# Optimization experiments

Measured on AMD Instinct MI355X. Metric: run time of the kernel, lower is better.

The kernel has to match this reference:

```python
import jax, jax.numpy as jnp
import numpy as np

N_HEAD = 16


def _rope(x, cos, sin):
    # x: [B, T, H, hd]; cos/sin: [1, T, 1, hd//2] (interleaved-pair rotation)
    x1, x2 = x[..., ::2], x[..., 1::2]
    r1 = x1 * cos - x2 * sin
    r2 = x1 * sin + x2 * cos
    return jnp.stack([r1, r2], axis=-1).reshape(x.shape)


def setup_inputs() -> dict:
    key = jax.random.key(0)
    k1, k2, k3 = jax.random.split(key, 3)
    B, T, D = 2, 2048, 2048
    x = jax.random.normal(k1, (B, T, D), dtype=jnp.float32)
    w_attn = jax.random.normal(k2, (3 * D, D), dtype=jnp.float32) * 0.02
    w_proj = jax.random.normal(k3, (D, D), dtype=jnp.float32) * 0.02
    return {"x": x, "w_attn": w_attn, "w_proj": w_proj}


def reference(x, w_attn, w_proj):
    B, T, D = x.shape
    H = N_HEAD
    hd = D // H
    # fused QKV projection (bias=False)
    qkv = x @ w_attn.T                      # [B, T, 3D]
    q, k, v = jnp.split(qkv, 3, axis=-1)
    q = q.reshape(B, T, H, hd)
    k = k.reshape(B, T, H, hd)
    v = v.reshape(B, T, H, hd)
    # RoPE tables: inv_freq = 1/10000^(2i/hd), angles m*theta_i
    inv_freq = 1.0 / (10000.0 ** (jnp.arange(0, hd, 2, dtype=jnp.float32) / hd))
    t = jnp.arange(T, dtype=jnp.float32)
    freqs = t[:, None] * inv_freq[None, :]  # [T, hd//2]
    cos = jnp.cos(freqs)[None, :, None, :]
    sin = jnp.sin(freqs)[None, :, None, :]
    q = _rope(q, cos, sin)
    k = _rope(k, cos, sin)
    # causal attention with materialized [B,H,T,T] scores (as in source)
    scale = 1.0 / np.sqrt(hd).astype(np.float32)
    att = jnp.einsum('bthd,bshd->bhts', q, k) * scale
    causal = jnp.tril(jnp.ones((T, T), dtype=bool))
    att = jnp.where(causal, att, -jnp.inf)
    att = jax.nn.softmax(att, axis=-1)
    y = jnp.einsum('bhts,bshd->bthd', att, v).reshape(B, T, D)
    return y @ w_proj.T
```

## Files before the change

kernel.cpp:

```cpp
#include <hip/hip_runtime.h>
#include <hip/hip_bf16.h>

#define T_SEQ 2048
#define DMODEL 2048
#define NB 2
#define NH 16
#define HD 128

typedef __attribute__((ext_vector_type(8))) short short8;
typedef __attribute__((ext_vector_type(4))) float f32x4;
typedef __attribute__((ext_vector_type(16))) float f32x16;
typedef unsigned short ushort_t;

__device__ inline ushort_t f2bf(float f) {
  union { float f; unsigned u; } v; v.f = f;
  unsigned r = v.u + 0x7fffu + ((v.u >> 16) & 1u);
  return (ushort_t)(r >> 16);
}
__device__ inline float bf2f(ushort_t u) {
  union { unsigned u; float f; } v; v.u = ((unsigned)u) << 16;
  return v.f;
}
__device__ inline unsigned pk2(float x, float y) {
  union { __hip_bfloat162 h; unsigned u; } c;
  c.h = __float22bfloat162_rn(float2{x, y});
  return c.u;
}
__device__ inline float fexp2(float x) {
  float r;
  asm("v_exp_f32 %0, %1" : "=v"(r) : "v"(x));
  return r;
}

__device__ inline void gload16(const void* g, void* l) {
  __builtin_amdgcn_global_load_lds(
      (const __attribute__((address_space(1))) unsigned*)g,
      (__attribute__((address_space(3))) unsigned*)l, 16, 0, 0);
}

__global__ void cvt_all(const float* __restrict__ x, const float* __restrict__ wa,
                        const float* __restrict__ wp, ushort_t* __restrict__ xb,
                        ushort_t* __restrict__ wab, ushort_t* __restrict__ wpb,
                        int n8x, int n8a, int n8p) {
  int i = blockIdx.x * blockDim.x + threadIdx.x;
  const float* src; ushort_t* dst; int j;
  if (i < n8x)              { src = x;  dst = xb;  j = i; }
  else if (i < n8x + n8a)   { src = wa; dst = wab; j = i - n8x; }
  else if (i < n8x + n8a + n8p) { src = wp; dst = wpb; j = i - n8x - n8a; }
  else return;
  const float4* s = (const float4*)src + (size_t)j * 2;
  float4 a = s[0], b = s[1];
  short8 o;
  o[0] = (short)f2bf(a.x); o[1] = (short)f2bf(a.y);
  o[2] = (short)f2bf(a.z); o[3] = (short)f2bf(a.w);
  o[4] = (short)f2bf(b.x); o[5] = (short)f2bf(b.y);
  o[6] = (short)f2bf(b.z); o[7] = (short)f2bf(b.w);
  *((short8*)dst + j) = o;
}

__global__ void trig_init(float* __restrict__ trig) {
  int idx = blockIdx.x * blockDim.x + threadIdx.x;
  if (idx >= T_SEQ * 64) return;
  int i = idx & 63, t = idx >> 6;
  float inv = __expf(-(float)i * (9.210340371976184f / 64.0f));
  float f = (float)t * inv;
  trig[idx * 2]     = cosf(f);
  trig[idx * 2 + 1] = sinf(f);
}

__global__ __launch_bounds__(256)
void v_transpose(const ushort_t* __restrict__ v, ushort_t* __restrict__ vt) {
  __shared__ __align__(16) ushort_t L[64][136];
  int bh = blockIdx.y;
  int t0 = blockIdx.x * 64;
  int tid = threadIdx.x;
  int row = tid >> 2, c0 = (tid & 3) * 32;
  const ushort_t* src = v + ((size_t)bh * T_SEQ + t0 + row) * HD + c0;
#pragma unroll
  for (int j = 0; j < 4; ++j)
    *(short8*)&L[row][c0 + j * 8] = *(const short8*)(src + j * 8);
  __syncthreads();
  int d = tid >> 1, tc = (tid & 1) * 32;
  union { ushort_t u[32]; short8 v8[4]; } buf;
#pragma unroll
  for (int j = 0; j < 32; ++j) buf.u[j] = L[tc + j][d];
  ushort_t* dst = vt + ((size_t)bh * HD + d) * T_SEQ + t0 + tc;
#pragma unroll
  for (int j = 0; j < 4; ++j) *(short8*)(dst + j * 8) = buf.v8[j];
}

template <int EPI>
__global__ __launch_bounds__(256, 4)
void gemm_s(const ushort_t* __restrict__ A, const ushort_t* __restrict__ Bt,
            float* __restrict__ C, ushort_t* __restrict__ q_t,
            ushort_t* __restrict__ k_t, ushort_t* __restrict__ v_t,
            const float* __restrict__ trig, int M, int N, int K) {
  __shared__ __align__(16) ushort_t sA[2][128 * 32];
  __shared__ __align__(16) ushort_t sB[2][128 * 32];
  int tid = threadIdx.x, lane = tid & 63, w = tid >> 6;
  int wm = w >> 1, wn = w & 1;
  int li = lane & 15, lg = lane >> 4;
  int tile_m = blockIdx.y * 128, tile_n = blockIdx.x * 128;
  const ushort_t* Ag = A + (size_t)tile_m * K;
  const ushort_t* Bg = Bt + (size_t)tile_n * K;

  int Rl = tid >> 3;
  int sl = tid & 7;
  int tdec = sl ^ (Rl & 7);
  int prow = (tdec >> 2) & 1, gch = tdec & 3;

  auto stage = [&](int kt, int buf) {
#pragma unroll
    for (int i = 0; i < 2; ++i) {
      int grow = (i * 32 + Rl) * 2 + prow;
      gload16(Ag + (size_t)grow * K + kt * 32 + gch * 8,
              &sA[buf][i * 2048 + tid * 8]);
    }
#pragma unroll
    for (int i = 0; i < 2; ++i) {
      int grow = (i * 32 + Rl) * 2 + prow;
      gload16(Bg + (size_t)grow * K + kt * 32 + gch * 8,
              &sB[buf][i * 2048 + tid * 8]);
    }
  };

  auto rdoff = [&](int r) {
    int R = r >> 1;
    int s = (((r & 1) << 2) | lg) ^ (R & 7);
    return R * 64 + s * 8;
  };

  f32x4 acc[4][4] = {};
  const int NT = K / 32;

  stage(0, 0);
  __syncthreads();

  for (int kt = 0; kt < NT; ++kt) {
    int cur = kt & 1;
    if (kt + 1 < NT) stage(kt + 1, cur ^ 1);
    short8 af[4], bf[4];
#pragma unroll
    for (int mi = 0; mi < 4; ++mi)
      af[mi] = *(const short8*)&sA[cur][rdoff(wm * 64 + mi * 16 + li)];
#pragma unroll
    for (int ni = 0; ni < 4; ++ni)
      bf[ni] = *(const short8*)&sB[cur][rdoff(wn * 64 + ni * 16 + li)];
    __builtin_amdgcn_s_setprio(1);
#pragma unroll
    for (int mi = 0; mi < 4; ++mi)
#pragma unroll
      for (int ni = 0; ni < 4; ++ni)
        acc[mi][ni] = __builtin_amdgcn_mfma_f32_16x16x32_bf16(af[mi], bf[ni], acc[mi][ni], 0, 0, 0);
    __builtin_amdgcn_s_setprio(0);
    __syncthreads();
  }

  if (EPI == 0) {
#pragma unroll
    for (int mi = 0; mi < 4; ++mi) {
      int trow = tile_m + wm * 64 + mi * 16 + lg * 4;
#pragma unroll
      for (int ni = 0; ni < 4; ++ni) {
        int col = tile_n + wn * 64 + ni * 16 + li;
#pragma unroll
        for (int r = 0; r < 4; ++r)
          C[(size_t)(trow + r) * N + col] = acc[mi][ni][r];
      }
    }
  } else {
    int sec = tile_n >> 11;
    int bq  = tile_m >> 11;
    int t0  = tile_m & 2047;
    int h   = (tile_n & 2047) >> 7;
#pragma unroll
    for (int mi = 0; mi < 4; ++mi) {
      int tl = wm * 64 + mi * 16 + lg * 4;
#pragma unroll
      for (int ni = 0; ni < 4; ++ni) {
        int d = wn * 64 + ni * 16 + li;
        if (sec < 2) {
          ushort_t* base = ((sec == 0) ? q_t : k_t) + ((size_t)(bq * NH + h)) * T_SEQ * HD;
          int fi2 = (d >> 1) * 2;
#pragma unroll
          for (int r = 0; r < 4; ++r) {
            int t = t0 + tl + r;
            float val = acc[mi][ni][r];
            float par = __shfl_xor(val, 1);
            const float* tp = trig + t * 128 + fi2;
            float c = tp[0], s = tp[1];
            float outv = (li & 1) ? (par * s + val * c) : (val * c - par * s);
            base[(size_t)t * HD + d] = f2bf(outv);
          }
        } else {
          ushort_t* base = v_t + ((size_t)(bq * NH + h)) * T_SEQ * HD;
#pragma unroll
          for (int r = 0; r < 4; ++r)
            base[(size_t)(t0 + tl + r) * HD + d] = f2bf(acc[mi][ni][r]);
        }
      }
    }
  }
}

__global__ __launch_bounds__(256, 2)
void flash_attn(const ushort_t* __restrict__ Q, const ushort_t* __restrict__ Kg,
                const ushort_t* __restrict__ Vt, ushort_t* __restrict__ Y) {
  __shared__ __align__(16) ushort_t ldsK[2 * 64 * 128];
  __shared__ __align__(16) ushort_t ldsV[2 * 128 * 64];
  int tid = threadIdx.x, lane = tid & 63, w = tid >> 6;
  int hi = lane >> 5, l31 = lane & 31;
  int qi = (blockIdx.y & 16) ? (15 - (int)blockIdx.x) : (int)blockIdx.x;
  int bh = blockIdx.y;
  int b = bh >> 4, h = bh & 15;
  int q0 = qi * 128;
  const ushort_t* Qp = Q + (size_t)bh * T_SEQ * HD;
  const ushort_t* Kp = Kg + (size_t)bh * T_SEQ * HD;
  const ushort_t* Vp = Vt + (size_t)bh * HD * T_SEQ;

  int qg = q0 + w * 32 + l31;
  int qmaxw = q0 + w * 32 + 31;

  auto stage = [&](int kv0, int bsel) {
    ushort_t* Kb = ldsK + bsel * 8192;
    ushort_t* Vb = ldsV + bsel * 8192;
#pragma unroll
    for (int p = 0; p < 4; ++p) {
      int c = p * 256 + w * 64 + lane;
      {
        int row = c >> 4, cc = c & 15;
        int sc = cc ^ (row & 15);
        gload16(Kp + (size_t)(kv0 + row) * HD + sc * 8, Kb + (p * 256 + w * 64) * 8);
      }
      {
        int d = c >> 3, cc = c & 7;
        int sc = cc ^ (d & 7);
        gload16(Vp + (size_t)d * T_SEQ + kv0 + sc * 8, Vb + (p * 256 + w * 64) * 8);
      }
    }
  };

  short8 qf[8];
#pragma unroll
  for (int ds = 0; ds < 8; ++ds)
    qf[ds] = *(const short8*)(Qp + (size_t)qg * HD + ds * 16 + hi * 8);

  f32x16 o[4] = {};
  float mu = -1e30f, l = 0.f;
  const float SIG = 0.12751879523209784f;

  int nkt = 2 * qi + 2;
  stage(0, 0);
  __syncthreads();
  int cur = 0;
  for (int kt = 0; kt < nkt; ++kt) {
    int kv0 = kt * 64;
    if (kt + 1 < nkt) stage((kt + 1) * 64, cur ^ 1);
    if (kv0 <= qmaxw) {
      const ushort_t* Kb = ldsK + cur * 8192;
      const ushort_t* Vb = ldsV + cur * 8192;
      f32x16 sa = {}, sb = {};
      __builtin_amdgcn_s_setprio(1);
#pragma unroll
      for (int ds = 0; ds < 8; ++ds) {
        int cc = ds * 2 + hi;
        short8 k0 = *(const short8*)&Kb[l31 * 128 + ((cc ^ (l31 & 15)) * 8)];
        short8 k1 = *(const short8*)&Kb[(32 + l31) * 128 + ((cc ^ (l31 & 15)) * 8)];
        sa = __builtin_amdgcn_mfma_f32_32x32x16_bf16(k0, qf[ds], sa, 0, 0, 0);
        sb = __builtin_amdgcn_mfma_f32_32x32x16_bf16(k1, qf[ds], sb, 0, 0, 0);
      }
      __builtin_amdgcn_s_setprio(0);
      float p[32];
#pragma unroll
      for (int r = 0; r < 16; ++r) { p[r] = sa[r] * SIG; p[16 + r] = sb[r] * SIG; }
      if (kv0 + 63 > q0 + w * 32) {
#pragma unroll
        for (int r = 0; r < 16; ++r) {
          int loc = (r & 3) + 8 * (r >> 2) + 4 * hi;
          if (kv0 + loc > qg)      p[r]      = -3e38f;
          if (kv0 + 32 + loc > qg) p[16 + r] = -3e38f;
        }
      }
      float tm[16];
#pragma unroll
      for (int i = 0; i < 16; ++i) tm[i] = fmaxf(p[i], p[i + 16]);
#pragma unroll
      for (int st = 8; st >= 1; st >>= 1)
#pragma unroll
        for (int i = 0; i < 8; ++i)
          if (i < st) tm[i] = fmaxf(tm[i], tm[i + st]);
      float pmax = fmaxf(tm[0], __shfl_xor(tm[0], 32));
      bool resc = !__all(pmax <= mu + 11.0f);
      if (resc) {
        float munew = fmaxf(mu, pmax);
        float alpha = fexp2(mu - munew);
        mu = munew;
        l *= alpha;
#pragma unroll
        for (int dsub = 0; dsub < 4; ++dsub)
#pragma unroll
          for (int r = 0; r < 16; ++r) o[dsub][r] *= alpha;
      }
#pragma unroll
      for (int i = 0; i < 32; ++i) p[i] = fexp2(p[i] - mu);
      float ts[16];
#pragma unroll
      for (int i = 0; i < 16; ++i) ts[i] = p[i] + p[i + 16];
#pragma unroll
      for (int st = 8; st >= 1; st >>= 1)
#pragma unroll
        for (int i = 0; i < 8; ++i)
          if (i < st) ts[i] += ts[i + st];
      l += ts[0] + __shfl_xor(ts[0], 32);
      __builtin_amdgcn_s_setprio(1);
#pragma unroll
      for (int s = 0; s < 4; ++s) {
        int rb = (s >> 1) * 16 + (s & 1) * 8;
        unsigned a0 = pk2(p[rb + 0], p[rb + 1]);
        unsigned a1 = pk2(p[rb + 2], p[rb + 3]);
        unsigned a2 = pk2(p[rb + 4], p[rb + 5]);
        unsigned a3 = pk2(p[rb + 6], p[rb + 7]);
        unsigned sa0 = (unsigned)__shfl_xor((int)a0, 32);
        unsigned sa1 = (unsigned)__shfl_xor((int)a1, 32);
        unsigned sa2 = (unsigned)__shfl_xor((int)a2, 32);
        unsigned sa3 = (unsigned)__shfl_xor((int)a3, 32);
        union { unsigned u[4]; short8 s8; } pf;
        pf.u[0] = hi ? sa2 : a0;
        pf.u[1] = hi ? sa3 : a1;
        pf.u[2] = hi ? a2 : sa0;
        pf.u[3] = hi ? a3 : sa1;
#pragma unroll
        for (int dsub = 0; dsub < 4; ++dsub) {
          int row = dsub * 32 + l31;
          short8 vf = *(const short8*)&Vb[row * 64 + (((2 * s + hi) ^ (row & 7)) * 8)];
          o[dsub] = __builtin_amdgcn_mfma_f32_32x32x16_bf16(vf, pf.s8, o[dsub], 0, 0, 0);
        }
      }
      __builtin_amdgcn_s_setprio(0);
    }
    __syncthreads();
    cur ^= 1;
  }
  float invl = 1.f / l;
#pragma unroll
  for (int dsub = 0; dsub < 4; ++dsub)
#pragma unroll
    for (int r = 0; r < 16; ++r) o[dsub][r] *= invl;
#pragma unroll
  for (int dsub = 0; dsub < 4; ++dsub)
#pragma unroll
    for (int r = 0; r < 16; r += 2) {
      int d0 = dsub * 32 + (r & 3) + 8 * (r >> 2) + 4 * hi;
      unsigned u = pk2(o[dsub][r], o[dsub][r + 1]);
      *(unsigned*)&ldsK[w * 4096 + l31 * 128 + (((d0 >> 3) ^ (l31 & 15)) * 8) + (d0 & 7)] = u;
    }
  __syncthreads();
#pragma unroll
  for (int rep = 0; rep < 8; ++rep) {
    int idx = rep * 256 + tid;
    int qg2 = idx >> 4, c = idx & 15;
    int wv2 = qg2 >> 5, ql = qg2 & 31;
    short8 val = *(const short8*)&ldsK[wv2 * 4096 + ql * 128 + ((c ^ (ql & 15)) * 8)];
    *(short8*)(Y + ((size_t)(b * T_SEQ + q0 + qg2)) * DMODEL + h * HD + c * 8) = val;
  }
}

extern "C" void kernel_launch(void* const* d_in, const int* in_sizes, int n_in,
                              void* d_out, int out_size, void* d_ws, size_t ws_size,
                              hipStream_t stream) {
  const float* x      = (const float*)d_in[0];
  const float* w_attn = (const float*)d_in[1];
  const float* w_proj = (const float*)d_in[2];
  float* out = (float*)d_out;

  char* ws = (char*)d_ws;
  size_t off = 0;
  auto alloc = [&](size_t bytes) -> void* {
    void* p = ws + off;
    off = (off + bytes + 255) & ~(size_t)255;
    return p;
  };
  const size_t MT = (size_t)NB * T_SEQ;
  ushort_t* xb   = (ushort_t*)alloc(MT * DMODEL * 2);
  ushort_t* wab  = (ushort_t*)alloc((size_t)3 * DMODEL * DMODEL * 2);
  ushort_t* wpb  = (ushort_t*)alloc((size_t)DMODEL * DMODEL * 2);
  ushort_t* q_t  = (ushort_t*)alloc(MT * DMODEL * 2);
  ushort_t* k_t  = (ushort_t*)alloc(MT * DMODEL * 2);
  ushort_t* v_t  = (ushort_t*)alloc(MT * DMODEL * 2);
  ushort_t* vtb  = (ushort_t*)alloc(MT * DMODEL * 2);
  ushort_t* yb   = (ushort_t*)alloc(MT * DMODEL * 2);
  float*    trig = (float*)alloc((size_t)T_SEQ * 64 * 2 * 4);
  (void)ws_size; (void)n_in; (void)in_sizes; (void)out_size;

  {
    int n8x = (int)(MT * DMODEL / 8);
    int n8a = (int)((size_t)3 * DMODEL * DMODEL / 8);
    int n8p = (int)((size_t)DMODEL * DMODEL / 8);
    int tot = n8x + n8a + n8p;
    hipLaunchKernelGGL(cvt_all, dim3((tot + 255) / 256), dim3(256), 0, stream,
                       x, w_attn, w_proj, xb, wab, wpb, n8x, n8a, n8p);
  }
  hipLaunchKernelGGL(trig_init, dim3(T_SEQ * 64 / 256), dim3(256), 0, stream, trig);

  hipLaunchKernelGGL((gemm_s<1>), dim3(3 * DMODEL / 128, MT / 128), dim3(256), 0, stream,
                     xb, wab, (float*)nullptr, q_t, k_t, v_t, trig,
                     (int)MT, 3 * DMODEL, DMODEL);

  hipLaunchKernelGGL(v_transpose, dim3(T_SEQ / 64, NB * NH), dim3(256), 0, stream, v_t, vtb);

  hipLaunchKernelGGL(flash_attn, dim3(T_SEQ / 128, NB * NH), dim3(256), 0, stream,
                     q_t, k_t, vtb, yb);

  hipLaunchKernelGGL((gemm_s<0>), dim3(DMODEL / 128, MT / 128), dim3(256), 0, stream,
                     yb, wpb, out, (ushort_t*)nullptr, (ushort_t*)nullptr, (ushort_t*)nullptr,
                     (const float*)nullptr, (int)MT, DMODEL, DMODEL);
}
```

Baseline: 294.7 us.

## Fuse V transpose into QKV GEMM epilogue and enlarge GEMM tiles to 256x128

The QKV GEMM epilogue now writes V directly in transposed [d][t] layout through a shared-memory staging buffer, which removes the separate v_transpose kernel and its extra global round trip. Both GEMMs also move to 512-thread blocks with 256x128 output tiles, giving more A-tile reuse per B load and fewer blocks. The costs are extra barriers in the V epilogue, more LDS per block and lower occupancy, plus some tail-wave risk from having fewer blocks.

```diff
diff --git a/kernel.cpp b/kernel.cpp
--- a/kernel.cpp
+++ b/kernel.cpp
@@ -68,39 +68,18 @@
   trig[idx * 2 + 1] = sinf(f);
 }
 
-__global__ __launch_bounds__(256)
-void v_transpose(const ushort_t* __restrict__ v, ushort_t* __restrict__ vt) {
-  __shared__ __align__(16) ushort_t L[64][136];
-  int bh = blockIdx.y;
-  int t0 = blockIdx.x * 64;
-  int tid = threadIdx.x;
-  int row = tid >> 2, c0 = (tid & 3) * 32;
-  const ushort_t* src = v + ((size_t)bh * T_SEQ + t0 + row) * HD + c0;
-#pragma unroll
-  for (int j = 0; j < 4; ++j)
-    *(short8*)&L[row][c0 + j * 8] = *(const short8*)(src + j * 8);
-  __syncthreads();
-  int d = tid >> 1, tc = (tid & 1) * 32;
-  union { ushort_t u[32]; short8 v8[4]; } buf;
-#pragma unroll
-  for (int j = 0; j < 32; ++j) buf.u[j] = L[tc + j][d];
-  ushort_t* dst = vt + ((size_t)bh * HD + d) * T_SEQ + t0 + tc;
-#pragma unroll
-  for (int j = 0; j < 4; ++j) *(short8*)(dst + j * 8) = buf.v8[j];
-}
-
 template <int EPI>
-__global__ __launch_bounds__(256, 4)
+__global__ __launch_bounds__(512, 4)
 void gemm_s(const ushort_t* __restrict__ A, const ushort_t* __restrict__ Bt,
             float* __restrict__ C, ushort_t* __restrict__ q_t,
             ushort_t* __restrict__ k_t, ushort_t* __restrict__ v_t,
             const float* __restrict__ trig, int M, int N, int K) {
-  __shared__ __align__(16) ushort_t sA[2][128 * 32];
+  __shared__ __align__(16) ushort_t sA[2][256 * 32];
   __shared__ __align__(16) ushort_t sB[2][128 * 32];
   int tid = threadIdx.x, lane = tid & 63, w = tid >> 6;
   int wm = w >> 1, wn = w & 1;
   int li = lane & 15, lg = lane >> 4;
-  int tile_m = blockIdx.y * 128, tile_n = blockIdx.x * 128;
+  int tile_m = blockIdx.y * 256, tile_n = blockIdx.x * 128;
   const ushort_t* Ag = A + (size_t)tile_m * K;
   const ushort_t* Bg = Bt + (size_t)tile_n * K;
 
@@ -112,15 +91,14 @@
   auto stage = [&](int kt, int buf) {
 #pragma unroll
     for (int i = 0; i < 2; ++i) {
-      int grow = (i * 32 + Rl) * 2 + prow;
+      int grow = (i * 64 + Rl) * 2 + prow;
       gload16(Ag + (size_t)grow * K + kt * 32 + gch * 8,
-              &sA[buf][i * 2048 + tid * 8]);
-    }
-#pragma unroll
-    for (int i = 0; i < 2; ++i) {
-      int grow = (i * 32 + Rl) * 2 + prow;
+              &sA[buf][i * 4096 + tid * 8]);
+    }
+    {
+      int grow = Rl * 2 + prow;
       gload16(Bg + (size_t)grow * K + kt * 32 + gch * 8,
-              &sB[buf][i * 2048 + tid * 8]);
+              &sB[buf][tid * 8]);
     }
   };
 
@@ -173,14 +151,14 @@
     int bq  = tile_m >> 11;
     int t0  = tile_m & 2047;
     int h   = (tile_n & 2047) >> 7;
-#pragma unroll
-    for (int mi = 0; mi < 4; ++mi) {
-      int tl = wm * 64 + mi * 16 + lg * 4;
-#pragma unroll
-      for (int ni = 0; ni < 4; ++ni) {
-        int d = wn * 64 + ni * 16 + li;
-        if (sec < 2) {
-          ushort_t* base = ((sec == 0) ? q_t : k_t) + ((size_t)(bq * NH + h)) * T_SEQ * HD;
+    if (sec < 2) {
+      ushort_t* base = ((sec == 0) ? q_t : k_t) + ((size_t)(bq * NH + h)) * T_SEQ * HD;
+#pragma unroll
+      for (int mi = 0; mi < 4; ++mi) {
+        int tl = wm * 64 + mi * 16 + lg * 4;
+#pragma unroll
+        for (int ni = 0; ni < 4; ++ni) {
+          int d = wn * 64 + ni * 16 + li;
           int fi2 = (d >> 1) * 2;
 #pragma unroll
           for (int r = 0; r < 4; ++r) {
@@ -192,12 +170,34 @@
             float outv = (li & 1) ? (par * s + val * c) : (val * c - par * s);
             base[(size_t)t * HD + d] = f2bf(outv);
           }
-        } else {
-          ushort_t* base = v_t + ((size_t)(bq * NH + h)) * T_SEQ * HD;
-#pragma unroll
-          for (int r = 0; r < 4; ++r)
-            base[(size_t)(t0 + tl + r) * HD + d] = f2bf(acc[mi][ni][r]);
         }
+      }
+    } else {
+      ushort_t* vbase = v_t + ((size_t)(bq * NH + h)) * HD * T_SEQ;
+      ushort_t* L = (ushort_t*)sA;
+      for (int c = 0; c < 4; ++c) {
+        if (wm == c) {
+#pragma unroll
+          for (int mi = 0; mi < 4; ++mi) {
+            int tl = mi * 16 + lg * 4;
+#pragma unroll
+            for (int ni = 0; ni < 4; ++ni) {
+              int d = wn * 64 + ni * 16 + li;
+#pragma unroll
+              for (int r = 0; r < 4; ++r)
+                L[d * 72 + tl + r] = f2bf(acc[mi][ni][r]);
+            }
+          }
+        }
+        __syncthreads();
+#pragma unroll
+        for (int j = 0; j < 2; ++j) {
+          int idx = j * 512 + tid;
+          int d = idx >> 3, tg = (idx & 7) * 8;
+          short8 val = *(const short8*)&L[d * 72 + tg];
+          *(short8*)(vbase + (size_t)d * T_SEQ + t0 + c * 64 + tg) = val;
+        }
+        __syncthreads();
       }
     }
   }
@@ -386,7 +386,6 @@
   ushort_t* wpb  = (ushort_t*)alloc((size_t)DMODEL * DMODEL * 2);
   ushort_t* q_t  = (ushort_t*)alloc(MT * DMODEL * 2);
   ushort_t* k_t  = (ushort_t*)alloc(MT * DMODEL * 2);
-  ushort_t* v_t  = (ushort_t*)alloc(MT * DMODEL * 2);
   ushort_t* vtb  = (ushort_t*)alloc(MT * DMODEL * 2);
   ushort_t* yb   = (ushort_t*)alloc(MT * DMODEL * 2);
   float*    trig = (float*)alloc((size_t)T_SEQ * 64 * 2 * 4);
@@ -402,16 +401,14 @@
   }
   hipLaunchKernelGGL(trig_init, dim3(T_SEQ * 64 / 256), dim3(256), 0, stream, trig);
 
-  hipLaunchKernelGGL((gemm_s<1>), dim3(3 * DMODEL / 128, MT / 128), dim3(256), 0, stream,
-                     xb, wab, (float*)nullptr, q_t, k_t, v_t, trig,
+  hipLaunchKernelGGL((gemm_s<1>), dim3(3 * DMODEL / 128, MT / 256), dim3(512), 0, stream,
+                     xb, wab, (float*)nullptr, q_t, k_t, vtb, trig,
                      (int)MT, 3 * DMODEL, DMODEL);
-
-  hipLaunchKernelGGL(v_transpose, dim3(T_SEQ / 64, NB * NH), dim3(256), 0, stream, v_t, vtb);
 
   hipLaunchKernelGGL(flash_attn, dim3(T_SEQ / 128, NB * NH), dim3(256), 0, stream,
                      q_t, k_t, vtb, yb);
 
-  hipLaunchKernelGGL((gemm_s<0>), dim3(DMODEL / 128, MT / 128), dim3(256), 0, stream,
+  hipLaunchKernelGGL((gemm_s<0>), dim3(DMODEL / 128, MT / 256), dim3(512), 0, stream,
                      yb, wpb, out, (ushort_t*)nullptr, (ushort_t*)nullptr, (ushort_t*)nullptr,
                      (const float*)nullptr, (int)MT, DMODEL, DMODEL);
 }
```

Result: faster. 279.2 us (-5.3%).
